# Kernel tuning notes

Measured on AMD Instinct MI355X. Metric: run time of the kernel, lower is better.

The kernel has to match this reference:

```python
import jax, jax.numpy as jnp
import numpy as np

EMBED_DIM = 1024
NUM_HEADS = 16
HEAD_DIM = EMBED_DIM // NUM_HEADS
TGT_LEN = 1024
SRC_LEN = 1024
BSZ = 4


def setup_inputs() -> dict:
    key = jax.random.key(0)
    ks = jax.random.split(key, 7)
    query = jax.random.normal(ks[0], (TGT_LEN, BSZ, EMBED_DIM), dtype=jnp.float32)
    key_t = jax.random.normal(ks[1], (SRC_LEN, BSZ, EMBED_DIM), dtype=jnp.float32)
    # hard 0/1 multiplicative mask applied post-softmax
    hard_attention = jax.random.randint(ks[2], (BSZ, TGT_LEN, SRC_LEN), 0, 2).astype(jnp.float32)
    # xavier_uniform_ on [3E, E]
    limit = float(np.sqrt(6.0 / (3 * EMBED_DIM + EMBED_DIM)))
    in_proj_weight = jax.random.uniform(ks[3], (3 * EMBED_DIM, EMBED_DIM), dtype=jnp.float32,
                                        minval=-limit, maxval=limit)
    in_proj_bias = jnp.zeros((3 * EMBED_DIM,), dtype=jnp.float32)
    limit_o = float(np.sqrt(1.0 / EMBED_DIM))
    out_proj_weight = jax.random.uniform(ks[4], (EMBED_DIM, EMBED_DIM), dtype=jnp.float32,
                                         minval=-limit_o, maxval=limit_o)
    out_proj_bias = jnp.zeros((EMBED_DIM,), dtype=jnp.float32)
    return {
        "query": query,
        "key": key_t,
        "hard_attention": hard_attention,
        "in_proj_weight": in_proj_weight,
        "in_proj_bias": in_proj_bias,
        "out_proj_weight": out_proj_weight,
        "out_proj_bias": out_proj_bias,
    }


def reference(query, key, hard_attention, in_proj_weight, in_proj_bias,
              out_proj_weight, out_proj_bias):
    tgt_len, bsz, embed_dim = query.shape
    src_len = key.shape[0]
    h, hd = NUM_HEADS, embed_dim // NUM_HEADS
    scaling = float(hd) ** -0.5

    # QKV projections (F.linear uses y = x @ W.T + b)
    wq = in_proj_weight[:embed_dim]
    wkv = in_proj_weight[embed_dim:]
    bq = in_proj_bias[:embed_dim]
    bkv = in_proj_bias[embed_dim:]
    q = jnp.einsum('tbe,fe->tbf', query, wq) + bq          # [T,B,E]
    kv = jnp.einsum('sbe,fe->sbf', key, wkv) + bkv          # [S,B,2E]
    k, v = jnp.split(kv, 2, axis=-1)

    q = (q * scaling).reshape(tgt_len, bsz, h, hd).transpose(1, 2, 0, 3)  # [B,H,T,D]
    k = k.reshape(src_len, bsz, h, hd).transpose(1, 2, 0, 3)              # [B,H,S,D]
    v = v.reshape(src_len, bsz, h, hd).transpose(1, 2, 0, 3)              # [B,H,S,D]

    scores = jnp.einsum('bhtd,bhsd->bhts', q, k)            # [B,H,T,S]
    attn = jax.nn.softmax(scores, axis=-1)
    # dropout_p = 0.0 -> identity
    attn = attn * hard_attention[:, None, :, :]             # post-softmax hard mask

    out = jnp.einsum('bhts,bhsd->bhtd', attn, v)            # [B,H,T,D]
    out = out.transpose(2, 0, 1, 3).reshape(tgt_len, bsz, embed_dim)
    out = jnp.einsum('tbe,fe->tbf', out, out_proj_weight) + out_proj_bias

    avg_weights = attn.sum(axis=1) / h                      # [B,T,S]
    return (out, avg_weights)
```

## Files before the change

### kernel.cpp

```cpp
#include <hip/hip_runtime.h>
#include <cstdint>
#include <cstddef>

typedef __bf16 bf16x8 __attribute__((ext_vector_type(8)));
typedef float  f32x4  __attribute__((ext_vector_type(4)));
typedef unsigned short u16x8 __attribute__((ext_vector_type(8)));

__device__ __forceinline__ uint16_t f2bf(float f) {
  uint32_t u = __float_as_uint(f);
  u += 0x7fffu + ((u >> 16) & 1u);
  return (uint16_t)(u >> 16);
}
__device__ __forceinline__ float bf2f(uint16_t u) {
  return __uint_as_float((uint32_t)u << 16);
}
__device__ __forceinline__ uint32_t cvtpk(float lo, float hi) {
  uint32_t r;
  asm("v_cvt_pk_bf16_f32 %0, %1, %2" : "=v"(r) : "v"(lo), "v"(hi));
  return r;
}

__device__ __forceinline__ f32x4 mfma16(bf16x8 a, bf16x8 b, f32x4 c) {
  return __builtin_amdgcn_mfma_f32_16x16x32_bf16(a, b, c, 0, 0, 0);
}

#define GLD_TO_LDS16(gptr, lptr)                                                   \
  __builtin_amdgcn_global_load_lds(                                                \
      (const __attribute__((address_space(1))) void*)(gptr),                       \
      (__attribute__((address_space(3))) void*)(lptr), 16, 0, 0)

__global__ void prep(const float* __restrict__ q, const float* __restrict__ k,
                     const float* __restrict__ w, const float* __restrict__ wo,
                     const float* __restrict__ hard,
                     uint16_t* __restrict__ Xq, uint16_t* __restrict__ Xk,
                     uint16_t* __restrict__ Wb, uint16_t* __restrict__ Wob,
                     uint32_t* __restrict__ bits) {
  const int bid = blockIdx.x;
  if (bid < 12288) {
    int i = bid * 256 + threadIdx.x;
    const float* src;
    uint16_t* dst;
    int off;
    if (i < 1048576)      { src = q;  dst = Xq;  off = i; }
    else if (i < 2097152) { src = k;  dst = Xk;  off = i - 1048576; }
    else if (i < 2883584) { src = w;  dst = Wb;  off = i - 2097152; }
    else                  { src = wo; dst = Wob; off = i - 2883584; }
    float4 v = ((const float4*)src)[off];
    ushort4 o;
    o.x = f2bf(v.x); o.y = f2bf(v.y); o.z = f2bf(v.z); o.w = f2bf(v.w);
    ((ushort4*)dst)[off] = o;
  } else {
    int i = (bid - 12288) * 256 + threadIdx.x;
    unsigned long long m = __ballot(hard[i] != 0.0f);
    if ((threadIdx.x & 63) == 0) {
      int wd = i >> 5;
      bits[wd]     = (uint32_t)m;
      bits[wd + 1] = (uint32_t)(m >> 32);
    }
  }
}

__global__ __launch_bounds__(256)
void gemm_qkv(const uint16_t* __restrict__ Xq, const uint16_t* __restrict__ Xk,
              const uint16_t* __restrict__ Wb, const float* __restrict__ ipb,
              uint16_t* __restrict__ Qb, uint16_t* __restrict__ Kb,
              uint16_t* __restrict__ Vt) {
  __shared__ __align__(16) uint16_t As[128 * 32];
  __shared__ __align__(16) uint16_t Bs[128 * 32];
  const int tid  = threadIdx.x;
  const int wave = tid >> 6, lane = tid & 63;
  const int quad = lane >> 4, l16 = lane & 15;

  const int swz = (blockIdx.x & 7) * 96 + (blockIdx.x >> 3);
  const uint16_t *A, *B;
  const float* bias;
  int bm, bn, mode;
  if (swz < 256) {
    mode = 0; A = Xq; B = Wb; bias = ipb;
    bm = swz >> 3; bn = swz & 7;
  } else {
    mode = 1; A = Xk; B = Wb + (1 << 20); bias = ipb + 1024;
    int t = swz - 256; bm = t >> 4; bn = t & 15;
  }
  const int wm = (wave >> 1) << 6, wn = (wave & 1) << 6;
  const int K = 1024;

  f32x4 acc[4][4] = {};

  for (int k0 = 0; k0 < K; k0 += 32) {
    __syncthreads();
#pragma unroll
    for (int j = 0; j < 2; j++) {
      int c   = wave * 128 + j * 64 + lane;
      int row = c >> 2, kc = c & 3;
      const uint16_t* ga = A + (size_t)(bm * 128 + row) * K + k0 + kc * 8;
      GLD_TO_LDS16(ga, As + (size_t)(wave * 128 + j * 64) * 8);
      const uint16_t* gb = B + (size_t)(bn * 128 + row) * K + k0 + kc * 8;
      GLD_TO_LDS16(gb, Bs + (size_t)(wave * 128 + j * 64) * 8);
    }
    __syncthreads();

    bf16x8 af[4], bfr[4];
#pragma unroll
    for (int i = 0; i < 4; i++) {
      af[i]  = *(const bf16x8*)(As + (wm + i * 16 + l16) * 32 + quad * 8);
      bfr[i] = *(const bf16x8*)(Bs + (wn + i * 16 + l16) * 32 + quad * 8);
    }
#pragma unroll
    for (int mi = 0; mi < 4; mi++)
#pragma unroll
      for (int ni = 0; ni < 4; ni++)
        acc[mi][ni] = mfma16(af[mi], bfr[ni], acc[mi][ni]);
  }

#pragma unroll
  for (int mi = 0; mi < 4; mi++)
#pragma unroll
    for (int ni = 0; ni < 4; ni++)
#pragma unroll
      for (int r = 0; r < 4; r++) {
        int gi = bm * 128 + wm + mi * 16 + quad * 4 + r;
        int gf = bn * 128 + wn + ni * 16 + l16;
        float c = acc[mi][ni][r] + bias[gf];
        if (mode == 0) {
          c *= 0.125f;
          int t = gi >> 2, b = gi & 3, h = gf >> 6, d = gf & 63;
          Qb[((((size_t)b * 16 + h) * 1024 + t) << 6) + d] = f2bf(c);
        } else {
          int s = gi >> 2, b = gi & 3;
          if (gf < 1024) {
            int h = gf >> 6, d = gf & 63;
            Kb[((((size_t)b * 16 + h) * 1024 + s) << 6) + d] = f2bf(c);
          } else {
            int fv = gf - 1024, h = fv >> 6, d = fv & 63;
            Vt[((((size_t)b * 16 + h) * 64 + d) << 10) + s] = f2bf(c);
          }
        }
      }
}

__global__ __launch_bounds__(256, 2)
void attn_kernel(const uint16_t* __restrict__ qb, const uint16_t* __restrict__ kb,
                 const uint16_t* __restrict__ vtb, const uint32_t* __restrict__ bits,
                 uint16_t* __restrict__ attn_out, float* __restrict__ rlout) {
  __shared__ __align__(16) uint16_t Ks[128 * 64];
  __shared__ __align__(16) uint16_t Vs[64 * 128];
  __shared__ __align__(16) uint16_t Pb[4 * 32 * 128];

  const int bid = blockIdx.x;
  const int xcd = bid & 7, j = bid >> 3;
  const int slab = xcd * 8 + (j >> 3);
  const int b = slab >> 4, h = slab & 15;
  const int t0 = (j & 7) << 7;
  const int tid = threadIdx.x, wave = tid >> 6, lane = tid & 63;
  const int quad = lane >> 4, l16 = lane & 15;
  const int sw = (l16 & 7) << 4;
  const size_t bh = (size_t)b * 16 + h;
  const int tw = t0 + wave * 32;
  const int ta = tw + l16, tb = ta + 16;
  char* PwA = (char*)(Pb + wave * (32 * 128)) + l16 * 256;
  char* PwB = PwA + 16 * 256;

  const uint16_t* qA = qb + ((bh << 10) + ta) * 64;
  bf16x8 aqA0 = *(const bf16x8*)(qA + quad * 8);
  bf16x8 aqA1 = *(const bf16x8*)(qA + 32 + quad * 8);
  bf16x8 aqB0 = *(const bf16x8*)(qA + 1024 + quad * 8);
  bf16x8 aqB1 = *(const bf16x8*)(qA + 1024 + 32 + quad * 8);

  f32x4 accA[4] = {}, accB[4] = {};
  float smA = 0.f, smB = 0.f;

  const int kr = tid >> 3, kc8 = tid & 7;
  const int vr = tid >> 4, vc16 = tid & 15;

  const uint32_t* bA = bits + (((size_t)(b << 10) + ta) << 5);
  const uint32_t* bB = bits + (((size_t)(b << 10) + tb) << 5);

  u16x8 kreg[4], vreg[4];
#pragma unroll
  for (int r = 0; r < 4; r++)
    kreg[r] = *(const u16x8*)(kb + (bh << 16) + (size_t)(r * 256 + tid) * 8);
#pragma unroll
  for (int r = 0; r < 4; r++)
    vreg[r] = *(const u16x8*)(vtb + (((bh << 6) + r * 16 + vr) << 10) + vc16 * 8);
  uint4 uA = *(const uint4*)bA;
  uint4 uB = *(const uint4*)bB;

  for (int sc = 0; sc < 8; sc++) {
    uint32_t wA[4] = {uA.x >> (quad * 4), uA.y >> (quad * 4),
                      uA.z >> (quad * 4), uA.w >> (quad * 4)};
    uint32_t wB[4] = {uB.x >> (quad * 4), uB.y >> (quad * 4),
                      uB.z >> (quad * 4), uB.w >> (quad * 4)};

    __syncthreads();
#pragma unroll
    for (int r = 0; r < 4; r++) {
      const int row = r * 32 + kr;
      *(u16x8*)((char*)Ks + row * 128 + ((kc8 * 16) ^ ((row & 7) << 4))) = kreg[r];
    }
#pragma unroll
    for (int r = 0; r < 4; r++) {
      const int row = r * 16 + vr;
      *(u16x8*)((char*)Vs + row * 256 + ((vc16 * 16) ^ ((row & 7) << 4))) = vreg[r];
    }
    __syncthreads();

    if (sc < 7) {
      const uint16_t* kbase = kb + (bh << 16) + (size_t)(sc + 1) * 8192;
#pragma unroll
      for (int r = 0; r < 4; r++)
        kreg[r] = *(const u16x8*)(kbase + (size_t)(r * 256 + tid) * 8);
#pragma unroll
      for (int r = 0; r < 4; r++)
        vreg[r] = *(const u16x8*)(vtb + (((bh << 6) + r * 16 + vr) << 10) +
                                  (sc + 1) * 128 + vc16 * 8);
      uA = *(const uint4*)(bA + (sc + 1) * 4);
      uB = *(const uint4*)(bB + (sc + 1) * 4);
    }

#pragma unroll
    for (int nn = 0; nn < 8; nn++) {
      const char* kbp = (const char*)Ks + (nn * 16 + l16) * 128;
      bf16x8 bk0 = *(const bf16x8*)(kbp + ((quad * 16) ^ sw));
      bf16x8 bk1 = *(const bf16x8*)(kbp + ((64 + quad * 16) ^ sw));
      f32x4 cA = {}, cB = {};
      cA = mfma16(bk0, aqA0, cA); cA = mfma16(bk1, aqA1, cA);
      cB = mfma16(bk0, aqB0, cB); cB = mfma16(bk1, aqB1, cB);
      const uint32_t mA = wA[nn >> 1] >> ((nn & 1) * 16);
      const uint32_t mB = wB[nn >> 1] >> ((nn & 1) * 16);
      float eA[4], eB[4];
#pragma unroll
      for (int r = 0; r < 4; r++) {
        eA[r] = __expf(cA[r]); smA += eA[r];
        eB[r] = __expf(cB[r]); smB += eB[r];
        eA[r] = ((mA >> r) & 1) ? eA[r] : 0.f;
        eB[r] = ((mB >> r) & 1) ? eB[r] : 0.f;
      }
      const int pc = (nn * 32 + quad * 8) ^ sw;
      *(uint2*)(PwA + pc) = make_uint2(cvtpk(eA[0], eA[1]), cvtpk(eA[2], eA[3]));
      *(uint2*)(PwB + pc) = make_uint2(cvtpk(eB[0], eB[1]), cvtpk(eB[2], eB[3]));
    }

#pragma unroll
    for (int kc = 0; kc < 4; kc++) {
      const int pcb = (kc * 64 + quad * 16) ^ sw;
      bf16x8 apA = *(const bf16x8*)(PwA + pcb);
      bf16x8 apB = *(const bf16x8*)(PwB + pcb);
#pragma unroll
      for (int dt = 0; dt < 4; dt++) {
        bf16x8 bv = *(const bf16x8*)((const char*)Vs + (dt * 16 + l16) * 256 +
                                     ((kc * 64 + quad * 16) ^ sw));
        accA[dt] = mfma16(bv, apA, accA[dt]);
        accB[dt] = mfma16(bv, apB, accB[dt]);
      }
    }
  }

  smA += __shfl_xor(smA, 16); smA += __shfl_xor(smA, 32);
  smB += __shfl_xor(smB, 16); smB += __shfl_xor(smB, 32);
  const float rlA = 1.0f / smA, rlB = 1.0f / smB;
  if (quad == 0) rlout[(bh << 10) + ta] = rlA;
  if (quad == 1) rlout[(bh << 10) + tb] = rlB;

#pragma unroll
  for (int dt = 0; dt < 4; dt++) {
    uint2 oA = make_uint2(cvtpk(accA[dt][0] * rlA, accA[dt][1] * rlA),
                          cvtpk(accA[dt][2] * rlA, accA[dt][3] * rlA));
    *(uint2*)(attn_out + ((size_t)(ta * 4 + b) << 10) + h * 64 + dt * 16 + quad * 4) = oA;
    uint2 oB = make_uint2(cvtpk(accB[dt][0] * rlB, accB[dt][1] * rlB),
                          cvtpk(accB[dt][2] * rlB, accB[dt][3] * rlB));
    *(uint2*)(attn_out + ((size_t)(tb * 4 + b) << 10) + h * 64 + dt * 16 + quad * 4) = oB;
  }
}

__global__ __launch_bounds__(256, 4)
void tail(const uint16_t* __restrict__ qb, const uint16_t* __restrict__ kb,
          const float* __restrict__ rlin, const float* __restrict__ hard,
          const uint16_t* __restrict__ Ao, const uint16_t* __restrict__ Bw,
          const float* __restrict__ opb,
          float* __restrict__ out, float* __restrict__ avgout) {
  __shared__ __align__(16) char smem[16384];
  const int bid = blockIdx.x;
  const int tid = threadIdx.x, wave = tid >> 6, lane = tid & 63;
  const int quad = lane >> 4, l16 = lane & 15;

  if (bid < 512) {
    uint16_t* Ks = (uint16_t*)smem;
    const int xcd = bid & 7, j = bid >> 3;
    const int b  = xcd >> 1;
    const int t0 = ((xcd & 1) * 8 + (j >> 3)) << 6;
    const int s0 = (j & 7) << 7;
    const int sw = (l16 & 7) << 4;
    const int tr = t0 + wave * 16 + l16;
    const int kr = tid >> 3, kc8 = tid & 7;

    float av[8][4] = {};

    u16x8 kreg[4];
    {
      const uint16_t* kb0 = kb + ((((size_t)b * 16) << 10) + s0) * 64;
#pragma unroll
      for (int r = 0; r < 4; r++)
        kreg[r] = *(const u16x8*)(kb0 + (size_t)(r * 256 + tid) * 8);
    }

    for (int hh = 0; hh < 16; hh++) {
      __syncthreads();
#pragma unroll
      for (int r = 0; r < 4; r++) {
        const int row = r * 32 + kr;
        *(u16x8*)((char*)Ks + row * 128 + ((kc8 * 16) ^ ((row & 7) << 4))) = kreg[r];
      }
      __syncthreads();
      if (hh < 15) {
        const uint16_t* kb2 = kb + ((((size_t)b * 16 + hh + 1) << 10) + s0) * 64;
#pragma unroll
        for (int r = 0; r < 4; r++)
          kreg[r] = *(const u16x8*)(kb2 + (size_t)(r * 256 + tid) * 8);
      }

      const size_t bh = (size_t)b * 16 + hh;
      const uint16_t* qrow = qb + ((bh << 10) + tr) * 64;
      bf16x8 aq0 = *(const bf16x8*)(qrow + quad * 8);
      bf16x8 aq1 = *(const bf16x8*)(qrow + 32 + quad * 8);
      const float rl = rlin[(bh << 10) + tr];

#pragma unroll
      for (int n = 0; n < 8; n++) {
        const char* kbp = (const char*)Ks + (n * 16 + l16) * 128;
        bf16x8 bk0 = *(const bf16x8*)(kbp + ((quad * 16) ^ sw));
        bf16x8 bk1 = *(const bf16x8*)(kbp + ((64 + quad * 16) ^ sw));
        f32x4 c = {};
        c = mfma16(bk0, aq0, c);
        c = mfma16(bk1, aq1, c);
#pragma unroll
        for (int r = 0; r < 4; r++) av[n][r] += __expf(c[r]) * rl;
      }
    }

    const float* hrow = hard + (((size_t)(b << 10) + tr) << 10) + s0 + quad * 4;
    float* orow = avgout + ((size_t)(b << 10) + tr) * 1024 + s0 + quad * 4;
#pragma unroll
    for (int n = 0; n < 8; n++) {
      float4 hm = *(const float4*)(hrow + n * 16);
      float4 f;
      f.x = av[n][0] * (hm.x != 0.f ? 0.0625f : 0.f);
      f.y = av[n][1] * (hm.y != 0.f ? 0.0625f : 0.f);
      f.z = av[n][2] * (hm.z != 0.f ? 0.0625f : 0.f);
      f.w = av[n][3] * (hm.w != 0.f ? 0.0625f : 0.f);
      *(float4*)(orow + n * 16) = f;
    }
  } else {
    uint16_t* As = (uint16_t*)smem;
    uint16_t* Bs = (uint16_t*)(smem + 4096);
    const int u = bid - 512;
    const int swz = (u & 7) * 64 + (u >> 3);
    const int bm = swz >> 3, bn = swz & 7;
    const int wm = (wave >> 1) << 5, wn = (wave & 1) << 6;
    const int K = 1024;

    f32x4 acc[2][4] = {};

    for (int k0 = 0; k0 < K; k0 += 32) {
      __syncthreads();
      {
        int c   = wave * 64 + lane;
        int row = c >> 2, kc = c & 3;
        const uint16_t* ga = Ao + (size_t)(bm * 64 + row) * K + k0 + kc * 8;
        GLD_TO_LDS16(ga, As + (size_t)(wave * 64) * 8);
      }
#pragma unroll
      for (int jj = 0; jj < 2; jj++) {
        int c   = wave * 128 + jj * 64 + lane;
        int row = c >> 2, kc = c & 3;
        const uint16_t* gb = Bw + (size_t)(bn * 128 + row) * K + k0 + kc * 8;
        GLD_TO_LDS16(gb, Bs + (size_t)(wave * 128 + jj * 64) * 8);
      }
      __syncthreads();

      bf16x8 af[2], bfr[4];
#pragma unroll
      for (int i = 0; i < 2; i++)
        af[i] = *(const bf16x8*)(As + (wm + i * 16 + l16) * 32 + quad * 8);
#pragma unroll
      for (int i = 0; i < 4; i++)
        bfr[i] = *(const bf16x8*)(Bs + (wn + i * 16 + l16) * 32 + quad * 8);
#pragma unroll
      for (int mi = 0; mi < 2; mi++)
#pragma unroll
        for (int ni = 0; ni < 4; ni++)
          acc[mi][ni] = mfma16(af[mi], bfr[ni], acc[mi][ni]);
    }

#pragma unroll
    for (int mi = 0; mi < 2; mi++)
#pragma unroll
      for (int ni = 0; ni < 4; ni++)
#pragma unroll
        for (int r = 0; r < 4; r++) {
          int gi = bm * 64 + wm + mi * 16 + quad * 4 + r;
          int gf = bn * 128 + wn + ni * 16 + l16;
          out[(size_t)gi * 1024 + gf] = acc[mi][ni][r] + opb[gf];
        }
  }
}

extern "C" void kernel_launch(void* const* d_in, const int* in_sizes, int n_in,
                              void* d_out, int out_size, void* d_ws, size_t ws_size,
                              hipStream_t stream) {
  const float* query = (const float*)d_in[0];
  const float* key   = (const float*)d_in[1];
  const float* hard  = (const float*)d_in[2];
  const float* ipw   = (const float*)d_in[3];
  const float* ipb   = (const float*)d_in[4];
  const float* opw   = (const float*)d_in[5];
  const float* opb   = (const float*)d_in[6];

  char* ws = (char*)d_ws;
  const size_t MB = 1ull << 20;
  uint16_t* Xq  = (uint16_t*)(ws + 0);
  uint16_t* Xk  = (uint16_t*)(ws + 8 * MB);
  uint16_t* Wb  = (uint16_t*)(ws + 16 * MB);
  uint16_t* Wob = (uint16_t*)(ws + 22 * MB);
  uint16_t* Qb  = (uint16_t*)(ws + 24 * MB);
  uint16_t* Kb  = (uint16_t*)(ws + 32 * MB);
  uint16_t* Vt  = (uint16_t*)(ws + 40 * MB);
  uint16_t* AO  = Xq;
  float*    rlws = (float*)(ws + 8 * MB);

  float* out = (float*)d_out;
  float* avg = out + 4194304;
  uint32_t* bits = (uint32_t*)out;

  prep<<<28672, 256, 0, stream>>>(query, key, ipw, opw, hard,
                                  Xq, Xk, Wb, Wob, bits);

  gemm_qkv<<<768, 256, 0, stream>>>(Xq, Xk, Wb, ipb, Qb, Kb, Vt);

  attn_kernel<<<512, 256, 0, stream>>>(Qb, Kb, Vt, bits, AO, rlws);

  tail<<<1024, 256, 0, stream>>>(Qb, Kb, rlws, hard, AO, Wob, opb, out, avg);
}
```

Measured before the change: 229.7 us.

## Widen QKV GEMM K-tile to 64 with XOR-swizzled LDS, coarsen mask-bit packing

The QKV projection GEMM now stages 64-element K slices per iteration instead of 32, halving the number of barrier pairs across the K loop. It stores them in LDS with an XOR swizzle on 16-byte chunks so the fragment reads avoid bank conflicts. Separately, each prep block that packs the hard mask into bits now handles four chunks of 256 elements, so fewer blocks are launched. The trade is double the LDS footprint per GEMM block and more fragment registers, which may reduce occupancy.

```diff
diff --git a/kernel.cpp b/kernel.cpp
--- a/kernel.cpp
+++ b/kernel.cpp
@@ -50,12 +50,16 @@
     o.x = f2bf(v.x); o.y = f2bf(v.y); o.z = f2bf(v.z); o.w = f2bf(v.w);
     ((ushort4*)dst)[off] = o;
   } else {
-    int i = (bid - 12288) * 256 + threadIdx.x;
-    unsigned long long m = __ballot(hard[i] != 0.0f);
-    if ((threadIdx.x & 63) == 0) {
-      int wd = i >> 5;
-      bits[wd]     = (uint32_t)m;
-      bits[wd + 1] = (uint32_t)(m >> 32);
+    int base = (bid - 12288) * 1024;
+#pragma unroll
+    for (int c = 0; c < 4; c++) {
+      int i = base + c * 256 + threadIdx.x;
+      unsigned long long m = __ballot(hard[i] != 0.0f);
+      if ((threadIdx.x & 63) == 0) {
+        int wd = i >> 5;
+        bits[wd]     = (uint32_t)m;
+        bits[wd + 1] = (uint32_t)(m >> 32);
+      }
     }
   }
 }
@@ -65,11 +69,12 @@
               const uint16_t* __restrict__ Wb, const float* __restrict__ ipb,
               uint16_t* __restrict__ Qb, uint16_t* __restrict__ Kb,
               uint16_t* __restrict__ Vt) {
-  __shared__ __align__(16) uint16_t As[128 * 32];
-  __shared__ __align__(16) uint16_t Bs[128 * 32];
+  __shared__ __align__(16) char As[128 * 128];
+  __shared__ __align__(16) char Bs[128 * 128];
   const int tid  = threadIdx.x;
   const int wave = tid >> 6, lane = tid & 63;
   const int quad = lane >> 4, l16 = lane & 15;
+  const int sw = (l16 & 7) << 4;
 
   const int swz = (blockIdx.x & 7) * 96 + (blockIdx.x >> 3);
   const uint16_t *A, *B;
@@ -83,34 +88,44 @@
     int t = swz - 256; bm = t >> 4; bn = t & 15;
   }
   const int wm = (wave >> 1) << 6, wn = (wave & 1) << 6;
-  const int K = 1024;
+
+  const int lrow = lane >> 3;
+  const int scol = ((lane & 7) ^ lrow) << 4;
+  const char* Ag = (const char*)A + (size_t)(bm * 128) * 2048;
+  const char* Bg = (const char*)B + (size_t)(bn * 128) * 2048;
 
   f32x4 acc[4][4] = {};
 
-  for (int k0 = 0; k0 < K; k0 += 32) {
+  for (int k0 = 0; k0 < 2048; k0 += 128) {
     __syncthreads();
 #pragma unroll
-    for (int j = 0; j < 2; j++) {
-      int c   = wave * 128 + j * 64 + lane;
-      int row = c >> 2, kc = c & 3;
-      const uint16_t* ga = A + (size_t)(bm * 128 + row) * K + k0 + kc * 8;
-      GLD_TO_LDS16(ga, As + (size_t)(wave * 128 + j * 64) * 8);
-      const uint16_t* gb = B + (size_t)(bn * 128 + row) * K + k0 + kc * 8;
-      GLD_TO_LDS16(gb, Bs + (size_t)(wave * 128 + j * 64) * 8);
+    for (int j = 0; j < 4; j++) {
+      const int rbase = j * 32 + wave * 8;
+      GLD_TO_LDS16(Ag + (size_t)(rbase + lrow) * 2048 + k0 + scol,
+                   As + rbase * 128);
+      GLD_TO_LDS16(Bg + (size_t)(rbase + lrow) * 2048 + k0 + scol,
+                   Bs + rbase * 128);
     }
     __syncthreads();
 
-    bf16x8 af[4], bfr[4];
+    bf16x8 af[4][2], bfr[4][2];
 #pragma unroll
     for (int i = 0; i < 4; i++) {
-      af[i]  = *(const bf16x8*)(As + (wm + i * 16 + l16) * 32 + quad * 8);
-      bfr[i] = *(const bf16x8*)(Bs + (wn + i * 16 + l16) * 32 + quad * 8);
-    }
-#pragma unroll
-    for (int mi = 0; mi < 4; mi++)
-#pragma unroll
-      for (int ni = 0; ni < 4; ni++)
-        acc[mi][ni] = mfma16(af[mi], bfr[ni], acc[mi][ni]);
+      const char* pa = As + (wm + i * 16 + l16) * 128;
+      const char* pb = Bs + (wn + i * 16 + l16) * 128;
+#pragma unroll
+      for (int ks = 0; ks < 2; ks++) {
+        af[i][ks]  = *(const bf16x8*)(pa + ((ks * 64 + quad * 16) ^ sw));
+        bfr[i][ks] = *(const bf16x8*)(pb + ((ks * 64 + quad * 16) ^ sw));
+      }
+    }
+#pragma unroll
+    for (int ks = 0; ks < 2; ks++)
+#pragma unroll
+      for (int mi = 0; mi < 4; mi++)
+#pragma unroll
+        for (int ni = 0; ni < 4; ni++)
+          acc[mi][ni] = mfma16(af[mi][ks], bfr[ni][ks], acc[mi][ni]);
   }
 
 #pragma unroll
@@ -432,7 +447,7 @@
   float* avg = out + 4194304;
   uint32_t* bits = (uint32_t*)out;
 
-  prep<<<28672, 256, 0, stream>>>(query, key, ipw, opw, hard,
+  prep<<<16384, 256, 0, stream>>>(query, key, ipw, opw, hard,
                                   Xq, Xk, Wb, Wob, bits);
 
   gemm_qkv<<<768, 256, 0, stream>>>(Xq, Xk, Wb, ipb, Qb, Kb, Vt);
```

New measurement: 227.6 us (median of 2 runs). Within noise of the previous version (-0.9%).
